# Kernel optimization log

Hardware: AMD Instinct MI355X
Metric: run time of the kernel (lower is better)

The kernel has to match this reference:

```python
import jax, jax.numpy as jnp
import numpy as np

CHUNK = 128  # intra-chunk causal block size for the chunked linear-attention scan


def setup_inputs() -> dict:
    key = jax.random.key(0)
    ks = jax.random.split(key, 7)
    B, H, N, D, F = 1, 24, 4096, 128, 256
    q = jax.random.normal(ks[0], (B, H, N, D), dtype=jnp.float32)
    k = jax.random.normal(ks[1], (B, H, N, D), dtype=jnp.float32)
    v = jax.random.normal(ks[2], (B, H, N, D), dtype=jnp.float32)
    # fan-in scaling so phi features / accumulated state stay numerically sane
    w1 = jax.random.normal(ks[3], (F, D), dtype=jnp.float32) * (D ** -0.5)
    b1 = jax.random.normal(ks[4], (F,), dtype=jnp.float32) * 0.02
    w2 = jax.random.normal(ks[5], (F, F), dtype=jnp.float32) * (F ** -0.5)
    b2 = jax.random.normal(ks[6], (F,), dtype=jnp.float32) * 0.02
    return {"q": q, "k": k, "v": v, "w1": w1, "b1": b1, "w2": w2, "b2": b2}


def _phi(x, w1, b1, w2, b2):
    # Linear(D->F) -> SiLU -> Linear(F->F)
    h = jax.nn.silu(jnp.einsum('bnd,fd->bnf', x, w1) + b1)
    return jnp.einsum('bnf,gf->bng', h, w2) + b2


def _causal_scan(qp, kp, vf):
    # out_t = q_t . (sum_{s<=t} k_s v_s^T) / (t+1), chunked parallel form.
    BH, N, F = qp.shape
    D = vf.shape[-1]
    C = CHUNK
    nC = N // C
    qc = qp.reshape(BH, nC, C, F).transpose(1, 0, 2, 3)  # [nC,BH,C,F]
    kc = kp.reshape(BH, nC, C, F).transpose(1, 0, 2, 3)
    vc = vf.reshape(BH, nC, C, D).transpose(1, 0, 2, 3)
    offsets = (jnp.arange(nC) * C).astype(qp.dtype)
    mask = jnp.tril(jnp.ones((C, C), dtype=qp.dtype))  # include diagonal
    pos = jnp.arange(1, C + 1, dtype=qp.dtype)

    def step(w, inp):
        qb, kb, vb, off = inp
        inter = jnp.einsum('bcf,bfd->bcd', qb, w)
        attn = jnp.einsum('bcf,bsf->bcs', qb, kb) * mask
        intra = jnp.einsum('bcs,bsd->bcd', attn, vb)
        counts = off + pos  # global (token_idx + 1)
        out = (inter + intra) / counts[None, :, None]
        w = w + jnp.einsum('bcf,bcd->bfd', kb, vb)
        return w, out

    w0 = jnp.zeros((BH, F, D), dtype=qp.dtype)
    _, outs = jax.lax.scan(step, w0, (qc, kc, vc, offsets))  # outs [nC,BH,C,D]
    return outs.transpose(1, 0, 2, 3).reshape(BH, N, D)


def reference(q, k, v, w1, b1, w2, b2):
    B, H, N, D = q.shape
    qf = q.reshape(B * H, N, D)
    kf = k.reshape(B * H, N, D)
    vf = v.reshape(B * H, N, D)
    qp = _phi(qf, w1, b1, w2, b2)
    kp = _phi(kf, w1, b1, w2, b2)
    out_fwd = _causal_scan(qp, kp, vf)
    out_rev = _causal_scan(qp[:, ::-1], kp[:, ::-1], vf[:, ::-1])[:, ::-1]
    return (out_fwd + out_rev).reshape(B, H, N, D)
```

## Files before the change

### kernel.cpp

```cpp
#include <hip/hip_runtime.h>


typedef __attribute__((ext_vector_type(8))) _Float16 f16x8;
typedef __attribute__((ext_vector_type(4))) _Float16 f16x4;
typedef __attribute__((ext_vector_type(4))) float f32x4;

#define MFMA16(a, b, c) __builtin_amdgcn_mfma_f32_16x16x32_f16((a), (b), (c), 0, 0, 0)

constexpr int BH   = 24;
constexpr int NSEQ = 4096;
constexpr int DD   = 128;
constexpr int FF   = 256;
constexpr int CHK  = 128;
constexpr int NC   = NSEQ / CHK;
constexpr int NROWS = BH * NSEQ;

__global__ void prep_kernel(const float* __restrict__ w1, const float* __restrict__ w2,
                            _Float16* __restrict__ w1h, _Float16* __restrict__ w2h) {
  int i = blockIdx.x * 256 + threadIdx.x;
  if (i < FF * DD) w1h[i] = (_Float16)w1[i];
  if (i < FF * FF) w2h[i] = (_Float16)w2[i];
}

__global__ void vt_kernel(const float* __restrict__ v, _Float16* __restrict__ vT) {
  __shared__ __align__(16) _Float16 lt[128][136];
  int blk = blockIdx.x;
  int c = blk & 31, bh = blk >> 5;
  const float* vc = v + ((size_t)bh * NSEQ + c * CHK) * DD;
  int tid = threadIdx.x;
#pragma unroll
  for (int it = 0; it < 16; ++it) {
    int flat = it * 1024 + tid * 4;
    int s = flat >> 7, d0 = flat & 127;
    float4 xv = *(const float4*)&vc[(size_t)s * DD + d0];
    lt[d0 + 0][s] = (_Float16)xv.x;
    lt[d0 + 1][s] = (_Float16)xv.y;
    lt[d0 + 2][s] = (_Float16)xv.z;
    lt[d0 + 3][s] = (_Float16)xv.w;
  }
  __syncthreads();
#pragma unroll
  for (int it = 0; it < 8; ++it) {
    int flat = it * 256 + tid;
    int d = flat >> 4, sg = flat & 15;
    *(f16x8*)&vT[((size_t)bh * DD + d) * NSEQ + c * CHK + sg * 8] =
        *(const f16x8*)&lt[d][sg * 8];
  }
}

__global__ __launch_bounds__(256, 4)
void phi_kernel(const float* __restrict__ q, const float* __restrict__ k,
                const float* __restrict__ b1, const float* __restrict__ b2,
                const _Float16* __restrict__ w1h, const _Float16* __restrict__ w2h,
                _Float16* __restrict__ qp, _Float16* __restrict__ kp) {
  __shared__ __align__(16) char smem[16896];
  _Float16 (*xs)[136] = (_Float16(*)[136])smem;
  _Float16 (*hs)[264] = (_Float16(*)[264])smem;
  _Float16 (*os)[264] = (_Float16(*)[264])smem;
  int blk = blockIdx.x;
  bool isk = blk & 1;
  int rb = (blk >> 1) * 32;
  const float* src = isk ? k : q;
  _Float16* dst = isk ? kp : qp;
  int tid = threadIdx.x;
  int lane = tid & 63, wv = tid >> 6, lr = lane & 15, lq = lane >> 4;
  int wn = wv;

  float bb1[4], bb2[4];
#pragma unroll
  for (int fn = 0; fn < 4; ++fn) {
    bb1[fn] = b1[wn * 64 + fn * 16 + lr];
    bb2[fn] = b2[wn * 64 + fn * 16 + lr];
  }

#pragma unroll
  for (int it = 0; it < 4; ++it) {
    int flat = it * 256 + tid;
    int r = flat >> 5, dg = flat & 31;
    float4 xv = *(const float4*)&src[(size_t)(rb + r) * DD + dg * 4];
    f16x4 hv = {(_Float16)xv.x, (_Float16)xv.y, (_Float16)xv.z, (_Float16)xv.w};
    *(f16x4*)&xs[r][dg * 4] = hv;
  }
  __syncthreads();

  f32x4 acc[2][4] = {};
#pragma unroll
  for (int ks = 0; ks < 4; ++ks) {
    f16x8 bv[4];
#pragma unroll
    for (int fn = 0; fn < 4; ++fn)
      bv[fn] = *(const f16x8*)&w1h[(size_t)(wn * 64 + fn * 16 + lr) * DD + ks * 32 + lq * 8];
    f16x8 av[2];
#pragma unroll
    for (int im = 0; im < 2; ++im)
      av[im] = *(const f16x8*)&xs[im * 16 + lr][ks * 32 + lq * 8];
#pragma unroll
    for (int fn = 0; fn < 4; ++fn)
#pragma unroll
      for (int im = 0; im < 2; ++im) acc[im][fn] = MFMA16(av[im], bv[fn], acc[im][fn]);
  }
  __syncthreads();

#pragma unroll
  for (int im = 0; im < 2; ++im)
#pragma unroll
    for (int fn = 0; fn < 4; ++fn) {
      int f = wn * 64 + fn * 16 + lr;
      int r0 = im * 16 + lq * 4;
#pragma unroll
      for (int r = 0; r < 4; ++r) {
        float xv = acc[im][fn][r] + bb1[fn];
        hs[r0 + r][f] = (_Float16)(xv * __builtin_amdgcn_rcpf(1.0f + __expf(-xv)));
      }
    }
  __syncthreads();

  f32x4 ac2[2][4] = {};
#pragma unroll
  for (int ks = 0; ks < 8; ++ks) {
    f16x8 bv[4];
#pragma unroll
    for (int fn = 0; fn < 4; ++fn)
      bv[fn] = *(const f16x8*)&w2h[(size_t)(wn * 64 + fn * 16 + lr) * FF + ks * 32 + lq * 8];
    f16x8 av[2];
#pragma unroll
    for (int im = 0; im < 2; ++im)
      av[im] = *(const f16x8*)&hs[im * 16 + lr][ks * 32 + lq * 8];
#pragma unroll
    for (int fn = 0; fn < 4; ++fn)
#pragma unroll
      for (int im = 0; im < 2; ++im) ac2[im][fn] = MFMA16(av[im], bv[fn], ac2[im][fn]);
  }
  __syncthreads();

#pragma unroll
  for (int im = 0; im < 2; ++im)
#pragma unroll
    for (int fn = 0; fn < 4; ++fn) {
      int g = wn * 64 + fn * 16 + lr;
      int r0 = im * 16 + lq * 4;
#pragma unroll
      for (int r = 0; r < 4; ++r)
        os[r0 + r][g] = (_Float16)(ac2[im][fn][r] + bb2[fn]);
    }
  __syncthreads();
#pragma unroll
  for (int it = 0; it < 4; ++it) {
    int flat = it * 256 + tid;
    int r = flat >> 5, cg = flat & 31;
    *(f16x8*)&dst[(size_t)(rb + r) * FF + cg * 8] = *(const f16x8*)&os[r][cg * 8];
  }
}

__global__ __launch_bounds__(512, 2)
void s_kernel(const _Float16* __restrict__ vT, const _Float16* __restrict__ kp,
              _Float16* __restrict__ S) {
  __shared__ __align__(16) _Float16 vt[128][136];
  __shared__ __align__(16) _Float16 kt[256][136];
  int blk = blockIdx.x;
  int c = blk & 31, bh = blk >> 5;
  int tid = threadIdx.x;
#pragma unroll
  for (int it = 0; it < 4; ++it) {
    int flat = it * 512 + tid;
    int d = flat >> 4, sg = flat & 15;
    *(f16x8*)&vt[d][sg * 8] = *(const f16x8*)&vT[((size_t)bh * DD + d) * NSEQ + c * CHK + sg * 8];
  }
#pragma unroll
  for (int it = 0; it < 8; ++it) {
    int flat = it * 512 + tid;
    int s = flat >> 5, fg = flat & 31;
    f16x8 kv = *(const f16x8*)&kp[((size_t)bh * NSEQ + c * CHK + s) * FF + fg * 8];
    int sw = (fg & 15) << 3;
#pragma unroll
    for (int j = 0; j < 8; ++j)
      kt[fg * 8 + j][s ^ sw] = kv[j];
  }
  __syncthreads();
  int lane = tid & 63, wv = tid >> 6, lr = lane & 15, lq = lane >> 4;
  int wmd = wv & 1, wnf = wv >> 1;
  f32x4 acc[4][4] = {};
#pragma unroll
  for (int ks = 0; ks < 4; ++ks) {
    f16x8 av[4];
#pragma unroll
    for (int im = 0; im < 4; ++im)
      av[im] = *(const f16x8*)&vt[wmd * 64 + im * 16 + lr][ks * 32 + lq * 8];
#pragma unroll
    for (int fn = 0; fn < 4; ++fn) {
      int F = wnf * 64 + fn * 16 + lr;
      f16x8 bv = *(const f16x8*)&kt[F][(ks * 32 + lq * 8) ^ (((F >> 3) & 15) << 3)];
#pragma unroll
      for (int im = 0; im < 4; ++im) acc[im][fn] = MFMA16(av[im], bv, acc[im][fn]);
    }
  }
  _Float16* Sp = S + ((size_t)bh * NC + c) * (size_t)(DD * FF);
#pragma unroll
  for (int im = 0; im < 4; ++im)
#pragma unroll
    for (int fn = 0; fn < 4; ++fn) {
      int f = wnf * 64 + fn * 16 + lr;
#pragma unroll
      for (int r = 0; r < 4; ++r) {
        int d = wmd * 64 + im * 16 + lq * 4 + r;
        Sp[(size_t)d * FF + f] = (_Float16)acc[im][fn][r];
      }
    }
}

__global__ void prefix_kernel(_Float16* S_Wr, _Float16* __restrict__ Wf) {
  size_t idx = (size_t)blockIdx.x * 256 + threadIdx.x;
  int bh = (int)(idx >> 15);
  int df = (int)(idx & 32767);
  size_t base = (size_t)bh * NC * 32768 + df;
  float vals[NC];
#pragma unroll
  for (int c = 0; c < NC; ++c) vals[c] = (float)S_Wr[base + (size_t)c * 32768];
  float run = 0.f;
#pragma unroll
  for (int c = 0; c < NC; ++c) { Wf[base + (size_t)c * 32768] = (_Float16)run; run += vals[c]; }
  run = 0.f;
#pragma unroll
  for (int c = NC - 1; c >= 0; --c) { S_Wr[base + (size_t)c * 32768] = (_Float16)run; run += vals[c]; }
}

__global__ __launch_bounds__(512, 2)
void scan_kernel(const _Float16* __restrict__ qp, const _Float16* __restrict__ kp,
                 const _Float16* __restrict__ vT, const _Float16* __restrict__ Wf,
                 const _Float16* __restrict__ Wr, float* __restrict__ out) {
  __shared__ __align__(16) _Float16 vt[128][136];
  __shared__ __align__(16) _Float16 P[128][136];
  int blk = blockIdx.x;
  int c = blk & 31, bh = blk >> 5;
  const _Float16* qpc = qp + ((size_t)bh * NSEQ + c * CHK) * FF;
  const _Float16* kpc = kp + ((size_t)bh * NSEQ + c * CHK) * FF;
  int tid = threadIdx.x, lane = tid & 63, wv = tid >> 6, lr = lane & 15, lq = lane >> 4;
  int wm = wv & 3, wn = wv >> 2;

  f16x8 aq[2][8];
#pragma unroll
  for (int im = 0; im < 2; ++im)
#pragma unroll
    for (int ks = 0; ks < 8; ++ks)
      aq[im][ks] = *(const f16x8*)&qpc[(size_t)(wm * 32 + im * 16 + lr) * FF + ks * 32 + lq * 8];
#pragma unroll
  for (int it = 0; it < 4; ++it) {
    int flat = it * 512 + tid;
    int d = flat >> 4, sg = flat & 15;
    *(f16x8*)&vt[d][sg * 8] = *(const f16x8*)&vT[((size_t)bh * DD + d) * NSEQ + c * CHK + sg * 8];
  }
  f16x8 bk[2][8];
#pragma unroll
  for (int ks = 0; ks < 8; ++ks)
    bk[0][ks] = *(const f16x8*)&kpc[(size_t)(wn * 64 + lr) * FF + ks * 32 + lq * 8];
  f32x4 pacc[2][4] = {};
#pragma unroll
  for (int j = 0; j < 4; ++j) {
    int cur = j & 1;
    if (j < 3)
#pragma unroll
      for (int ks = 0; ks < 8; ++ks)
        bk[cur ^ 1][ks] = *(const f16x8*)&kpc[(size_t)(wn * 64 + (j + 1) * 16 + lr) * FF + ks * 32 + lq * 8];
#pragma unroll
    for (int ks = 0; ks < 8; ++ks)
#pragma unroll
      for (int im = 0; im < 2; ++im)
        pacc[im][j] = MFMA16(aq[im][ks], bk[cur][ks], pacc[im][j]);
  }
#pragma unroll
  for (int im = 0; im < 2; ++im)
#pragma unroll
    for (int j = 0; j < 4; ++j)
#pragma unroll
      for (int r = 0; r < 4; ++r)
        P[wm * 32 + im * 16 + lq * 4 + r][wn * 64 + j * 16 + lr] = (_Float16)pacc[im][j][r];

  const _Float16* Wfc = Wf + ((size_t)bh * NC + c) * (size_t)(DD * FF);
  const _Float16* Wrc = Wr + ((size_t)bh * NC + c) * (size_t)(DD * FF);
  f16x8 bf[8], br[8];
#pragma unroll
  for (int ks = 0; ks < 8; ++ks) {
    int d = wn * 64 + lr;
    bf[ks] = *(const f16x8*)&Wfc[(size_t)d * FF + ks * 32 + lq * 8];
    br[ks] = *(const f16x8*)&Wrc[(size_t)d * FF + ks * 32 + lq * 8];
  }
  __syncthreads();

  f32x4 af[2][4] = {}, ar[2][4] = {};
#pragma unroll
  for (int jd = 0; jd < 4; ++jd) {
#pragma unroll
    for (int ks = 0; ks < 8; ++ks)
#pragma unroll
      for (int im = 0; im < 2; ++im) {
        af[im][jd] = MFMA16(aq[im][ks], bf[ks], af[im][jd]);
        ar[im][jd] = MFMA16(aq[im][ks], br[ks], ar[im][jd]);
      }
    if (jd < 3)
#pragma unroll
      for (int ks = 0; ks < 8; ++ks) {
        int d = wn * 64 + (jd + 1) * 16 + lr;
        bf[ks] = *(const f16x8*)&Wfc[(size_t)d * FF + ks * 32 + lq * 8];
        br[ks] = *(const f16x8*)&Wrc[(size_t)d * FF + ks * 32 + lq * 8];
      }
    {
      int ks = jd;
      f16x8 bv[4];
#pragma unroll
      for (int jd2 = 0; jd2 < 4; ++jd2)
        bv[jd2] = *(const f16x8*)&vt[wn * 64 + jd2 * 16 + lr][ks * 32 + lq * 8];
#pragma unroll
      for (int im = 0; im < 2; ++im) {
        int irow = wm * 32 + im * 16 + lr;
        f16x8 p = *(const f16x8*)&P[irow][ks * 32 + lq * 8];
        f16x8 pf = p, pr = p;
#pragma unroll
        for (int jj = 0; jj < 8; ++jj) {
          int s = ks * 32 + lq * 8 + jj;
          pf[jj] = (s <= irow) ? p[jj] : (_Float16)0.0f;
          pr[jj] = (s >= irow) ? p[jj] : (_Float16)0.0f;
        }
#pragma unroll
        for (int jd2 = 0; jd2 < 4; ++jd2) {
          af[im][jd2] = MFMA16(pf, bv[jd2], af[im][jd2]);
          ar[im][jd2] = MFMA16(pr, bv[jd2], ar[im][jd2]);
        }
      }
    }
  }

  float* oc = out + ((size_t)bh * NSEQ + c * CHK) * DD;
#pragma unroll
  for (int im = 0; im < 2; ++im)
#pragma unroll
    for (int jd = 0; jd < 4; ++jd) {
      int d = wn * 64 + jd * 16 + lr;
#pragma unroll
      for (int r = 0; r < 4; ++r) {
        int il = wm * 32 + im * 16 + lq * 4 + r;
        int gi = c * CHK + il;
        oc[(size_t)il * DD + d] = af[im][jd][r] / (float)(gi + 1) + ar[im][jd][r] / (float)(NSEQ - gi);
      }
    }
}

extern "C" void kernel_launch(void* const* d_in, const int* in_sizes, int n_in,
                              void* d_out, int out_size, void* d_ws, size_t ws_size,
                              hipStream_t stream) {
  const float* q  = (const float*)d_in[0];
  const float* k  = (const float*)d_in[1];
  const float* v  = (const float*)d_in[2];
  const float* w1 = (const float*)d_in[3];
  const float* b1 = (const float*)d_in[4];
  const float* w2 = (const float*)d_in[5];
  const float* b2 = (const float*)d_in[6];
  float* out = (float*)d_out;

  char* ws = (char*)d_ws;
  const size_t SZ = 50331648ull;
  _Float16* w1h = (_Float16*)(ws);
  _Float16* w2h = (_Float16*)(ws + 65536);
  _Float16* qp  = (_Float16*)(ws + 196608);
  _Float16* kp  = (_Float16*)(ws + 196608 + SZ);
  _Float16* Wf  = (_Float16*)(ws + 196608 + 2 * SZ);
  _Float16* S   = (_Float16*)(ws + 196608 + 3 * SZ);
  _Float16* vT  = (_Float16*)(ws + 196608 + 4 * SZ);
  _Float16* Wr  = S;

  prep_kernel<<<dim3(256), dim3(256), 0, stream>>>(w1, w2, w1h, w2h);
  vt_kernel<<<dim3(BH * NC), dim3(256), 0, stream>>>(v, vT);
  phi_kernel<<<dim3(2 * NROWS / 32), dim3(256), 0, stream>>>(q, k, b1, b2, w1h, w2h, qp, kp);
  s_kernel<<<dim3(BH * NC), dim3(512), 0, stream>>>(vT, kp, S);
  prefix_kernel<<<dim3(BH * DD * FF / 256), dim3(256), 0, stream>>>(S, Wf);
  scan_kernel<<<dim3(BH * NC), dim3(512), 0, stream>>>(qp, kp, vT, Wf, Wr, out);
}
```

Measured before the change: 445.2 us.

## Double phi kernel row tile and software-pipeline weight fragment loads

The phi MLP kernel now handles 64 rows per block with 512 threads: waves split two ways over rows and four ways over features, so each weight fragment fetched from global memory feeds twice as many rows. Weight B-fragments are double-buffered in registers (A/B sets) so the next k-step's loads are issued while the current MFMAs run, hiding global load latency. The cost is doubled shared memory and higher register pressure, which under launch_bounds(512,4) could lower occupancy or cause spills.

```diff
diff --git a/kernel.cpp b/kernel.cpp
--- a/kernel.cpp
+++ b/kernel.cpp
@@ -48,23 +48,33 @@
   }
 }
 
-__global__ __launch_bounds__(256, 4)
+__global__ __launch_bounds__(512, 4)
 void phi_kernel(const float* __restrict__ q, const float* __restrict__ k,
                 const float* __restrict__ b1, const float* __restrict__ b2,
                 const _Float16* __restrict__ w1h, const _Float16* __restrict__ w2h,
                 _Float16* __restrict__ qp, _Float16* __restrict__ kp) {
-  __shared__ __align__(16) char smem[16896];
+  __shared__ __align__(16) char smem[33792];
   _Float16 (*xs)[136] = (_Float16(*)[136])smem;
   _Float16 (*hs)[264] = (_Float16(*)[264])smem;
   _Float16 (*os)[264] = (_Float16(*)[264])smem;
   int blk = blockIdx.x;
   bool isk = blk & 1;
-  int rb = (blk >> 1) * 32;
+  int rb = (blk >> 1) * 64;
   const float* src = isk ? k : q;
   _Float16* dst = isk ? kp : qp;
   int tid = threadIdx.x;
   int lane = tid & 63, wv = tid >> 6, lr = lane & 15, lq = lane >> 4;
-  int wn = wv;
+  int wm = wv & 1, wn = wv >> 1;
+
+  const _Float16* w1row = w1h + (size_t)(wn * 64 + lr) * DD + lq * 8;
+  const _Float16* w2row = w2h + (size_t)(wn * 64 + lr) * FF + lq * 8;
+
+  f16x8 bwA[4], bwB[4];
+#pragma unroll
+  for (int fn = 0; fn < 4; ++fn) {
+    bwA[fn] = *(const f16x8*)&w1row[(size_t)(fn * 16) * DD + 0 * 32];
+    bwB[fn] = *(const f16x8*)&w1row[(size_t)(fn * 16) * DD + 1 * 32];
+  }
 
   float bb1[4], bb2[4];
 #pragma unroll
@@ -75,7 +85,7 @@
 
 #pragma unroll
   for (int it = 0; it < 4; ++it) {
-    int flat = it * 256 + tid;
+    int flat = it * 512 + tid;
     int r = flat >> 5, dg = flat & 31;
     float4 xv = *(const float4*)&src[(size_t)(rb + r) * DD + dg * 4];
     f16x4 hv = {(_Float16)xv.x, (_Float16)xv.y, (_Float16)xv.z, (_Float16)xv.w};
@@ -85,28 +95,51 @@
 
   f32x4 acc[2][4] = {};
 #pragma unroll
-  for (int ks = 0; ks < 4; ++ks) {
-    f16x8 bv[4];
-#pragma unroll
-    for (int fn = 0; fn < 4; ++fn)
-      bv[fn] = *(const f16x8*)&w1h[(size_t)(wn * 64 + fn * 16 + lr) * DD + ks * 32 + lq * 8];
-    f16x8 av[2];
-#pragma unroll
-    for (int im = 0; im < 2; ++im)
-      av[im] = *(const f16x8*)&xs[im * 16 + lr][ks * 32 + lq * 8];
-#pragma unroll
-    for (int fn = 0; fn < 4; ++fn)
-#pragma unroll
-      for (int im = 0; im < 2; ++im) acc[im][fn] = MFMA16(av[im], bv[fn], acc[im][fn]);
-  }
-  __syncthreads();
+  for (int p = 0; p < 2; ++p) {
+    {
+      f16x8 av[2];
+#pragma unroll
+      for (int im = 0; im < 2; ++im)
+        av[im] = *(const f16x8*)&xs[wm * 32 + im * 16 + lr][(2 * p) * 32 + lq * 8];
+#pragma unroll
+      for (int fn = 0; fn < 4; ++fn)
+#pragma unroll
+        for (int im = 0; im < 2; ++im) acc[im][fn] = MFMA16(av[im], bwA[fn], acc[im][fn]);
+      if (p < 1)
+#pragma unroll
+        for (int fn = 0; fn < 4; ++fn)
+          bwA[fn] = *(const f16x8*)&w1row[(size_t)(fn * 16) * DD + (2 * p + 2) * 32];
+    }
+    {
+      f16x8 av[2];
+#pragma unroll
+      for (int im = 0; im < 2; ++im)
+        av[im] = *(const f16x8*)&xs[wm * 32 + im * 16 + lr][(2 * p + 1) * 32 + lq * 8];
+#pragma unroll
+      for (int fn = 0; fn < 4; ++fn)
+#pragma unroll
+        for (int im = 0; im < 2; ++im) acc[im][fn] = MFMA16(av[im], bwB[fn], acc[im][fn]);
+      if (p < 1)
+#pragma unroll
+        for (int fn = 0; fn < 4; ++fn)
+          bwB[fn] = *(const f16x8*)&w1row[(size_t)(fn * 16) * DD + (2 * p + 3) * 32];
+    }
+  }
+  __syncthreads();
+
+  f16x8 cwA[4], cwB[4];
+#pragma unroll
+  for (int fn = 0; fn < 4; ++fn) {
+    cwA[fn] = *(const f16x8*)&w2row[(size_t)(fn * 16) * FF + 0 * 32];
+    cwB[fn] = *(const f16x8*)&w2row[(size_t)(fn * 16) * FF + 1 * 32];
+  }
 
 #pragma unroll
   for (int im = 0; im < 2; ++im)
 #pragma unroll
     for (int fn = 0; fn < 4; ++fn) {
       int f = wn * 64 + fn * 16 + lr;
-      int r0 = im * 16 + lq * 4;
+      int r0 = wm * 32 + im * 16 + lq * 4;
 #pragma unroll
       for (int r = 0; r < 4; ++r) {
         float xv = acc[im][fn][r] + bb1[fn];
@@ -117,19 +150,35 @@
 
   f32x4 ac2[2][4] = {};
 #pragma unroll
-  for (int ks = 0; ks < 8; ++ks) {
-    f16x8 bv[4];
-#pragma unroll
-    for (int fn = 0; fn < 4; ++fn)
-      bv[fn] = *(const f16x8*)&w2h[(size_t)(wn * 64 + fn * 16 + lr) * FF + ks * 32 + lq * 8];
-    f16x8 av[2];
-#pragma unroll
-    for (int im = 0; im < 2; ++im)
-      av[im] = *(const f16x8*)&hs[im * 16 + lr][ks * 32 + lq * 8];
-#pragma unroll
-    for (int fn = 0; fn < 4; ++fn)
-#pragma unroll
-      for (int im = 0; im < 2; ++im) ac2[im][fn] = MFMA16(av[im], bv[fn], ac2[im][fn]);
+  for (int p = 0; p < 4; ++p) {
+    {
+      f16x8 av[2];
+#pragma unroll
+      for (int im = 0; im < 2; ++im)
+        av[im] = *(const f16x8*)&hs[wm * 32 + im * 16 + lr][(2 * p) * 32 + lq * 8];
+#pragma unroll
+      for (int fn = 0; fn < 4; ++fn)
+#pragma unroll
+        for (int im = 0; im < 2; ++im) ac2[im][fn] = MFMA16(av[im], cwA[fn], ac2[im][fn]);
+      if (p < 3)
+#pragma unroll
+        for (int fn = 0; fn < 4; ++fn)
+          cwA[fn] = *(const f16x8*)&w2row[(size_t)(fn * 16) * FF + (2 * p + 2) * 32];
+    }
+    {
+      f16x8 av[2];
+#pragma unroll
+      for (int im = 0; im < 2; ++im)
+        av[im] = *(const f16x8*)&hs[wm * 32 + im * 16 + lr][(2 * p + 1) * 32 + lq * 8];
+#pragma unroll
+      for (int fn = 0; fn < 4; ++fn)
+#pragma unroll
+        for (int im = 0; im < 2; ++im) ac2[im][fn] = MFMA16(av[im], cwB[fn], ac2[im][fn]);
+      if (p < 3)
+#pragma unroll
+        for (int fn = 0; fn < 4; ++fn)
+          cwB[fn] = *(const f16x8*)&w2row[(size_t)(fn * 16) * FF + (2 * p + 3) * 32];
+    }
   }
   __syncthreads();
 
@@ -138,7 +187,7 @@
 #pragma unroll
     for (int fn = 0; fn < 4; ++fn) {
       int g = wn * 64 + fn * 16 + lr;
-      int r0 = im * 16 + lq * 4;
+      int r0 = wm * 32 + im * 16 + lq * 4;
 #pragma unroll
       for (int r = 0; r < 4; ++r)
         os[r0 + r][g] = (_Float16)(ac2[im][fn][r] + bb2[fn]);
@@ -146,7 +195,7 @@
   __syncthreads();
 #pragma unroll
   for (int it = 0; it < 4; ++it) {
-    int flat = it * 256 + tid;
+    int flat = it * 512 + tid;
     int r = flat >> 5, cg = flat & 31;
     *(f16x8*)&dst[(size_t)(rb + r) * FF + cg * 8] = *(const f16x8*)&os[r][cg * 8];
   }
@@ -369,7 +418,7 @@
 
   prep_kernel<<<dim3(256), dim3(256), 0, stream>>>(w1, w2, w1h, w2h);
   vt_kernel<<<dim3(BH * NC), dim3(256), 0, stream>>>(v, vT);
-  phi_kernel<<<dim3(2 * NROWS / 32), dim3(256), 0, stream>>>(q, k, b1, b2, w1h, w2h, qp, kp);
+  phi_kernel<<<dim3(2 * NROWS / 64), dim3(512), 0, stream>>>(q, k, b1, b2, w1h, w2h, qp, kp);
   s_kernel<<<dim3(BH * NC), dim3(512), 0, stream>>>(vT, kp, S);
   prefix_kernel<<<dim3(BH * DD * FF / 256), dim3(256), 0, stream>>>(S, Wf);
   scan_kernel<<<dim3(BH * NC), dim3(512), 0, stream>>>(qp, kp, vT, Wf, Wr, out);
```

Result: no change. 442.0 us (-0.7%).

## Split phi MLP into two persistent GEMM kernels with LDS-resident weights

Applied to the files above, without the earlier changes.

Replaces the fused per-32-row phi kernel with two persistent kernels of 256 blocks × 1024 threads. The first stages W1 in LDS and double-buffers input tiles to compute SiLU(xW1+b1) into an f16 scratch buffer. The second stages W2 in LDS and streams the hidden rows from global memory to produce qp/kp. The aim is to stop re-reading the weights from global/L2 for every small tile and to improve MFMA utilisation. The cost is an extra global write and read of the hidden activations, which reuse the Wf buffer, plus an extra launch.

```diff
diff --git a/kernel.cpp b/kernel.cpp
--- a/kernel.cpp
+++ b/kernel.cpp
@@ -48,107 +48,154 @@
   }
 }
 
-__global__ __launch_bounds__(256, 4)
-void phi_kernel(const float* __restrict__ q, const float* __restrict__ k,
-                const float* __restrict__ b1, const float* __restrict__ b2,
-                const _Float16* __restrict__ w1h, const _Float16* __restrict__ w2h,
-                _Float16* __restrict__ qp, _Float16* __restrict__ kp) {
-  __shared__ __align__(16) char smem[16896];
-  _Float16 (*xs)[136] = (_Float16(*)[136])smem;
-  _Float16 (*hs)[264] = (_Float16(*)[264])smem;
-  _Float16 (*os)[264] = (_Float16(*)[264])smem;
-  int blk = blockIdx.x;
-  bool isk = blk & 1;
-  int rb = (blk >> 1) * 32;
-  const float* src = isk ? k : q;
-  _Float16* dst = isk ? kp : qp;
+__global__ __launch_bounds__(1024, 4)
+void gemm1_kernel(const float* __restrict__ q, const float* __restrict__ k,
+                  const float* __restrict__ b1, const _Float16* __restrict__ w1h,
+                  _Float16* __restrict__ h) {
+  __shared__ __align__(16) _Float16 w1s[256][136];
+  __shared__ __align__(16) _Float16 xs[2][128][136];
   int tid = threadIdx.x;
   int lane = tid & 63, wv = tid >> 6, lr = lane & 15, lq = lane >> 4;
-  int wn = wv;
-
-  float bb1[4], bb2[4];
-#pragma unroll
-  for (int fn = 0; fn < 4; ++fn) {
-    bb1[fn] = b1[wn * 64 + fn * 16 + lr];
-    bb2[fn] = b2[wn * 64 + fn * 16 + lr];
-  }
+  int wm = wv & 3, wn = wv >> 2;
+  int blk = blockIdx.x;
+  const float* srcb = (blk < 128) ? q + (size_t)blk * 768 * DD
+                                  : k + (size_t)(blk - 128) * 768 * DD;
+  _Float16* hb = h + (size_t)blk * 768 * FF;
 
 #pragma unroll
   for (int it = 0; it < 4; ++it) {
-    int flat = it * 256 + tid;
+    int flat = it * 1024 + tid;
+    int f = flat >> 4, cg = flat & 15;
+    *(f16x8*)&w1s[f][cg * 8] = *(const f16x8*)&w1h[f * DD + cg * 8];
+  }
+#pragma unroll
+  for (int it = 0; it < 4; ++it) {
+    int flat = it * 1024 + tid;
     int r = flat >> 5, dg = flat & 31;
-    float4 xv = *(const float4*)&src[(size_t)(rb + r) * DD + dg * 4];
+    float4 xv = *(const float4*)&srcb[(size_t)r * DD + dg * 4];
     f16x4 hv = {(_Float16)xv.x, (_Float16)xv.y, (_Float16)xv.z, (_Float16)xv.w};
-    *(f16x4*)&xs[r][dg * 4] = hv;
-  }
+    *(f16x4*)&xs[0][r][dg * 4] = hv;
+  }
+  float bb1[4];
+#pragma unroll
+  for (int fn = 0; fn < 4; ++fn) bb1[fn] = b1[wn * 64 + fn * 16 + lr];
+
+  for (int t = 0; t < 6; ++t) {
+    int cur = t & 1;
+    __syncthreads();
+
+    float4 rx0, rx1, rx2, rx3;
+    if (t < 5) {
+      const float* nsrc = srcb + (size_t)(t + 1) * 128 * DD;
+      {int flat = 0 * 1024 + tid; rx0 = *(const float4*)&nsrc[(size_t)(flat >> 5) * DD + (flat & 31) * 4];}
+      {int flat = 1 * 1024 + tid; rx1 = *(const float4*)&nsrc[(size_t)(flat >> 5) * DD + (flat & 31) * 4];}
+      {int flat = 2 * 1024 + tid; rx2 = *(const float4*)&nsrc[(size_t)(flat >> 5) * DD + (flat & 31) * 4];}
+      {int flat = 3 * 1024 + tid; rx3 = *(const float4*)&nsrc[(size_t)(flat >> 5) * DD + (flat & 31) * 4];}
+    }
+
+    f32x4 acc[2][4] = {};
+#pragma unroll
+    for (int ks = 0; ks < 4; ++ks) {
+      f16x8 av[2];
+#pragma unroll
+      for (int im = 0; im < 2; ++im)
+        av[im] = *(const f16x8*)&xs[cur][wm * 32 + im * 16 + lr][ks * 32 + lq * 8];
+#pragma unroll
+      for (int fn = 0; fn < 4; ++fn) {
+        f16x8 bv = *(const f16x8*)&w1s[wn * 64 + fn * 16 + lr][ks * 32 + lq * 8];
+#pragma unroll
+        for (int im = 0; im < 2; ++im) acc[im][fn] = MFMA16(av[im], bv, acc[im][fn]);
+      }
+    }
+
+    _Float16* ht = hb + (size_t)t * 128 * FF;
+#pragma unroll
+    for (int im = 0; im < 2; ++im)
+#pragma unroll
+      for (int fn = 0; fn < 4; ++fn) {
+        int g = wn * 64 + fn * 16 + lr;
+        int r0 = wm * 32 + im * 16 + lq * 4;
+#pragma unroll
+        for (int r = 0; r < 4; ++r) {
+          float xv = acc[im][fn][r] + bb1[fn];
+          ht[(size_t)(r0 + r) * FF + g] = (_Float16)(xv * __builtin_amdgcn_rcpf(1.0f + __expf(-xv)));
+        }
+      }
+
+    if (t < 5) {
+      int nxt = cur ^ 1;
+      {int flat = 0 * 1024 + tid; f16x4 hv = {(_Float16)rx0.x, (_Float16)rx0.y, (_Float16)rx0.z, (_Float16)rx0.w};
+       *(f16x4*)&xs[nxt][flat >> 5][(flat & 31) * 4] = hv;}
+      {int flat = 1 * 1024 + tid; f16x4 hv = {(_Float16)rx1.x, (_Float16)rx1.y, (_Float16)rx1.z, (_Float16)rx1.w};
+       *(f16x4*)&xs[nxt][flat >> 5][(flat & 31) * 4] = hv;}
+      {int flat = 2 * 1024 + tid; f16x4 hv = {(_Float16)rx2.x, (_Float16)rx2.y, (_Float16)rx2.z, (_Float16)rx2.w};
+       *(f16x4*)&xs[nxt][flat >> 5][(flat & 31) * 4] = hv;}
+      {int flat = 3 * 1024 + tid; f16x4 hv = {(_Float16)rx3.x, (_Float16)rx3.y, (_Float16)rx3.z, (_Float16)rx3.w};
+       *(f16x4*)&xs[nxt][flat >> 5][(flat & 31) * 4] = hv;}
+    }
+  }
+}
+
+__global__ __launch_bounds__(1024, 4)
+void gemm2_kernel(const _Float16* __restrict__ h, const float* __restrict__ b2,
+                  const _Float16* __restrict__ w2h,
+                  _Float16* __restrict__ qp, _Float16* __restrict__ kp) {
+  __shared__ __align__(16) _Float16 w2s[256][264];
+  int tid = threadIdx.x;
+  int lane = tid & 63, wv = tid >> 6, lr = lane & 15, lq = lane >> 4;
+  int wm = wv & 3, wn = wv >> 2;
+  int blk = blockIdx.x;
+  const _Float16* hb = h + (size_t)blk * 768 * FF;
+  _Float16* dstb = (blk < 128) ? qp + (size_t)blk * 768 * FF
+                               : kp + (size_t)(blk - 128) * 768 * FF;
+
+#pragma unroll
+  for (int it = 0; it < 8; ++it) {
+    int flat = it * 1024 + tid;
+    int g = flat >> 5, cg = flat & 31;
+    *(f16x8*)&w2s[g][cg * 8] = *(const f16x8*)&w2h[(size_t)g * FF + cg * 8];
+  }
+  float bb2[4];
+#pragma unroll
+  for (int fn = 0; fn < 4; ++fn) bb2[fn] = b2[wn * 64 + fn * 16 + lr];
   __syncthreads();
 
-  f32x4 acc[2][4] = {};
-#pragma unroll
-  for (int ks = 0; ks < 4; ++ks) {
-    f16x8 bv[4];
-#pragma unroll
-    for (int fn = 0; fn < 4; ++fn)
-      bv[fn] = *(const f16x8*)&w1h[(size_t)(wn * 64 + fn * 16 + lr) * DD + ks * 32 + lq * 8];
-    f16x8 av[2];
+  auto loadA = [&](f16x8* av, int t, int im) {
+    const _Float16* p = hb + (size_t)(t * 128 + wm * 32 + im * 16 + lr) * FF + lq * 8;
+#pragma unroll
+    for (int ks = 0; ks < 8; ++ks) av[ks] = *(const f16x8*)&p[ks * 32];
+  };
+
+  f16x8 avA[8], avB[8];
+  loadA(avA, 0, 0);
+  for (int t = 0; t < 6; ++t) {
+    f32x4 acc[2][4] = {};
+    loadA(avB, t, 1);
+#pragma unroll
+    for (int ks = 0; ks < 8; ++ks)
+#pragma unroll
+      for (int fn = 0; fn < 4; ++fn) {
+        f16x8 bv = *(const f16x8*)&w2s[wn * 64 + fn * 16 + lr][ks * 32 + lq * 8];
+        acc[0][fn] = MFMA16(avA[ks], bv, acc[0][fn]);
+      }
+    if (t < 5) loadA(avA, t + 1, 0);
+#pragma unroll
+    for (int ks = 0; ks < 8; ++ks)
+#pragma unroll
+      for (int fn = 0; fn < 4; ++fn) {
+        f16x8 bv = *(const f16x8*)&w2s[wn * 64 + fn * 16 + lr][ks * 32 + lq * 8];
+        acc[1][fn] = MFMA16(avB[ks], bv, acc[1][fn]);
+      }
 #pragma unroll
     for (int im = 0; im < 2; ++im)
-      av[im] = *(const f16x8*)&xs[im * 16 + lr][ks * 32 + lq * 8];
-#pragma unroll
-    for (int fn = 0; fn < 4; ++fn)
-#pragma unroll
-      for (int im = 0; im < 2; ++im) acc[im][fn] = MFMA16(av[im], bv[fn], acc[im][fn]);
-  }
-  __syncthreads();
-
-#pragma unroll
-  for (int im = 0; im < 2; ++im)
-#pragma unroll
-    for (int fn = 0; fn < 4; ++fn) {
-      int f = wn * 64 + fn * 16 + lr;
-      int r0 = im * 16 + lq * 4;
-#pragma unroll
-      for (int r = 0; r < 4; ++r) {
-        float xv = acc[im][fn][r] + bb1[fn];
-        hs[r0 + r][f] = (_Float16)(xv * __builtin_amdgcn_rcpf(1.0f + __expf(-xv)));
-      }
-    }
-  __syncthreads();
-
-  f32x4 ac2[2][4] = {};
-#pragma unroll
-  for (int ks = 0; ks < 8; ++ks) {
-    f16x8 bv[4];
-#pragma unroll
-    for (int fn = 0; fn < 4; ++fn)
-      bv[fn] = *(const f16x8*)&w2h[(size_t)(wn * 64 + fn * 16 + lr) * FF + ks * 32 + lq * 8];
-    f16x8 av[2];
-#pragma unroll
-    for (int im = 0; im < 2; ++im)
-      av[im] = *(const f16x8*)&hs[im * 16 + lr][ks * 32 + lq * 8];
-#pragma unroll
-    for (int fn = 0; fn < 4; ++fn)
-#pragma unroll
-      for (int im = 0; im < 2; ++im) ac2[im][fn] = MFMA16(av[im], bv[fn], ac2[im][fn]);
-  }
-  __syncthreads();
-
-#pragma unroll
-  for (int im = 0; im < 2; ++im)
-#pragma unroll
-    for (int fn = 0; fn < 4; ++fn) {
-      int g = wn * 64 + fn * 16 + lr;
-      int r0 = im * 16 + lq * 4;
-#pragma unroll
-      for (int r = 0; r < 4; ++r)
-        os[r0 + r][g] = (_Float16)(ac2[im][fn][r] + bb2[fn]);
-    }
-  __syncthreads();
-#pragma unroll
-  for (int it = 0; it < 4; ++it) {
-    int flat = it * 256 + tid;
-    int r = flat >> 5, cg = flat & 31;
-    *(f16x8*)&dst[(size_t)(rb + r) * FF + cg * 8] = *(const f16x8*)&os[r][cg * 8];
+#pragma unroll
+      for (int fn = 0; fn < 4; ++fn) {
+        int g = wn * 64 + fn * 16 + lr;
+        int r0 = t * 128 + wm * 32 + im * 16 + lq * 4;
+#pragma unroll
+        for (int r = 0; r < 4; ++r)
+          dstb[(size_t)(r0 + r) * FF + g] = (_Float16)(acc[im][fn][r] + bb2[fn]);
+      }
   }
 }
 
@@ -366,10 +413,12 @@
   _Float16* S   = (_Float16*)(ws + 196608 + 3 * SZ);
   _Float16* vT  = (_Float16*)(ws + 196608 + 4 * SZ);
   _Float16* Wr  = S;
+  _Float16* h   = Wf;
 
   prep_kernel<<<dim3(256), dim3(256), 0, stream>>>(w1, w2, w1h, w2h);
   vt_kernel<<<dim3(BH * NC), dim3(256), 0, stream>>>(v, vT);
-  phi_kernel<<<dim3(2 * NROWS / 32), dim3(256), 0, stream>>>(q, k, b1, b2, w1h, w2h, qp, kp);
+  gemm1_kernel<<<dim3(256), dim3(1024), 0, stream>>>(q, k, b1, w1h, h);
+  gemm2_kernel<<<dim3(256), dim3(1024), 0, stream>>>(h, b2, w2h, qp, kp);
   s_kernel<<<dim3(BH * NC), dim3(512), 0, stream>>>(vT, kp, S);
   prefix_kernel<<<dim3(BH * DD * FF / 256), dim3(256), 0, stream>>>(S, Wf);
   scan_kernel<<<dim3(BH * NC), dim3(512), 0, stream>>>(qp, kp, vT, Wf, Wr, out);
```

Result: slower. 571.2 us (+28.3%).
